# Kernel tuning notes

Measured on AMD Instinct MI355X. Metric: run time of the kernel, lower is better.

## Reference

```python
import jax, jax.numpy as jnp
import numpy as np

D_MODEL = 1024
M = 64            # oscillators; state dim N = 2*M
N = 2 * M
N_H = 2           # Householder reflections per step
DT = 0.1
OMEGA_MAX = 100.0
BATCH, SEQ = 8, 2048


def setup_inputs() -> dict:
    key = jax.random.key(0)
    ks = jax.random.split(key, 8)
    u = jax.random.normal(ks[0], (BATCH, SEQ, D_MODEL), jnp.float32)
    # learned parameters (scaled like the module's small-gain init)
    W_A = jax.random.normal(ks[1], (M, D_MODEL), jnp.float32) * 0.01
    b_A = jnp.zeros((M,), jnp.float32)
    W_k = jax.random.normal(ks[2], (N_H, N, D_MODEL), jnp.float32) * 0.02
    b_k = jnp.zeros((N_H, N), jnp.float32)
    W_beta = jax.random.normal(ks[3], (N_H, D_MODEL), jnp.float32) * 0.02
    b_beta = jnp.zeros((N_H,), jnp.float32)
    B_w = jax.random.normal(ks[4], (N, D_MODEL), jnp.float32) * 0.02
    B_b = jnp.zeros((N,), jnp.float32)
    C = jax.random.normal(ks[5], (D_MODEL, N), jnp.float32) * 0.01
    D = jax.random.normal(ks[6], (D_MODEL,), jnp.float32) * 0.01
    return dict(u=u, W_A=W_A, b_A=b_A, W_k=W_k, b_k=b_k,
                W_beta=W_beta, b_beta=b_beta, B_w=B_w, B_b=B_b, C=C, D=D)


def reference(u, W_A, b_A, W_k, b_k, W_beta, b_beta, B_w, B_b, C, D):
    batch = u.shape[0]
    # --- precompute all input-dependent per-step quantities as big GEMMs ---
    A = jax.nn.relu(jnp.einsum('btd,md->btm', u, W_A) + b_A)
    A = jnp.minimum(A, OMEGA_MAX)                       # clamp(max=omega_max)
    S = 1.0 / (1.0 + (DT * DT) * A)                     # (B,T,M)
    K = jnp.einsum('btd,jnd->btjn', u, W_k) + b_k       # (B,T,n_h,N)
    K = K / jnp.maximum(jnp.linalg.norm(K, axis=-1, keepdims=True), 1e-12)
    beta = 2.0 * jax.nn.sigmoid(jnp.einsum('btd,jd->btj', u, W_beta) + b_beta)
    Bt = jnp.einsum('btd,nd->btn', u, B_w) + B_b        # (B,T,N)

    # time-major for scan
    xs = (jnp.moveaxis(A, 1, 0), jnp.moveaxis(S, 1, 0), jnp.moveaxis(K, 1, 0),
          jnp.moveaxis(beta, 1, 0), jnp.moveaxis(Bt, 1, 0))
    h0 = jnp.zeros((batch, N), u.dtype)

    def step(h, x):
        A_t, S_t, K_t, beta_t, B_t = x
        # oscillatory rotation-contraction R_t @ h (m 2x2 blocks)
        z, y = h[:, :M], h[:, M:]
        z_new = S_t * z - DT * A_t * S_t * y
        y_new = DT * S_t * z + S_t * y
        h = jnp.concatenate([z_new, y_new], axis=-1)
        # sequential Householder product H_t @ h (fixed small n_h loop)
        for j in range(N_H):
            k = K_t[:, j]                                # (B,N), unit norm
            dot = jnp.sum(k * h, axis=-1, keepdims=True)
            h = h - beta_t[:, j:j + 1] * k * dot
        h = h + B_t
        return h, h

    _, hs = jax.lax.scan(step, h0, xs)                  # (T,B,N)
    hs = jnp.moveaxis(hs, 0, 1)                         # (B,T,N)
    return jnp.einsum('btn,dn->btd', hs, C) + u * D
```

## Files before the change

### kernel.cpp

```cpp
#include <hip/hip_runtime.h>
#include <cmath>


#define NTOK 16384
#define TT 2048
#define BB 8
#define DM 1024
#define FS 520
#define CH 64
#define LCH 32
#define NCH 512
#define NW 448
#define NWP 512

typedef short bf16x8 __attribute__((ext_vector_type(8)));
typedef float f32x4 __attribute__((ext_vector_type(4)));

#define GLOAD_LDS16(g, l)                                          \
  __builtin_amdgcn_global_load_lds(                                \
      (const __attribute__((address_space(1))) void*)(g),          \
      (__attribute__((address_space(3))) void*)(l), 16, 0, 0)

__global__ __launch_bounds__(256) void packW(
    const float* __restrict__ W_A, const float* __restrict__ b_A,
    const float* __restrict__ W_k, const float* __restrict__ b_k,
    const float* __restrict__ b_beta,
    const float* __restrict__ B_w, const float* __restrict__ B_b,
    float* __restrict__ Wp, float* __restrict__ bias) {
  int r = blockIdx.x;
  int tid = threadIdx.x;
  const float* src;
  float bv;
  if (r < 64)       { src = W_A + (size_t)r * DM;         bv = b_A[r]; }
  else if (r < 320) { src = W_k + (size_t)(r - 64) * DM;  bv = b_k[r - 64]; }
  else              { src = B_w + (size_t)(r - 320) * DM; bv = B_b[r - 320]; }
  ((float4*)(Wp + (size_t)r * DM))[tid] = ((const float4*)src)[tid];
  if (tid == 0) bias[r] = bv;
  if (r == 0 && tid < 2) bias[448 + tid] = b_beta[tid];
}

__device__ inline unsigned short bf16_rne(float x) {
  unsigned b = __float_as_uint(x);
  b += 0x7FFFu + ((b >> 16) & 1u);
  return (unsigned short)(b >> 16);
}

__device__ inline void split_bf16(float x, unsigned short& h, unsigned short& l) {
  unsigned b = __float_as_uint(x);
  h = (unsigned short)(b >> 16);
  float rem = x - __uint_as_float(b & 0xFFFF0000u);
  l = bf16_rne(rem);
}

__global__ __launch_bounds__(256) void convertU(
    const float* __restrict__ u, unsigned short* __restrict__ uh,
    unsigned short* __restrict__ ul) {
  int gid = blockIdx.x * 256 + threadIdx.x;
  int m = gid >> 8;
  int g = gid & 255;
  float4 v = *(const float4*)(u + (size_t)m * DM + g * 4);
  int kt = g >> 3, gg = g & 7;
  int p = gg & 3, h = gg >> 2;
  int mr = m & 127, mb = m >> 7;
  int pp = p ^ ((mr >> 2) & 3);
  size_t dst = ((size_t)(mb * 32 + kt)) * 4096 + mr * 32 + ((pp << 1) | h) * 4;
  ushort4 hi, lo;
  split_bf16(v.x, hi.x, lo.x);
  split_bf16(v.y, hi.y, lo.y);
  split_bf16(v.z, hi.z, lo.z);
  split_bf16(v.w, hi.w, lo.w);
  *(ushort4*)(uh + dst) = hi;
  *(ushort4*)(ul + dst) = lo;
}

__global__ __launch_bounds__(256) void convertW(
    const float* __restrict__ Wp, unsigned short* __restrict__ Wb) {
  int gid = blockIdx.x * 256 + threadIdx.x;
  int n = gid >> 8, g = gid & 255;
  int kt = g >> 3, gg = g & 7;
  int p = gg & 3, h = gg >> 2;
  int nr = n & 127, nb = n >> 7;
  int pp = p ^ ((nr >> 2) & 3);
  size_t dst = ((size_t)(nb * 32 + kt)) * 4096 + nr * 32 + ((pp << 1) | h) * 4;
  ushort4 hv = make_ushort4(0, 0, 0, 0);
  if (n < NW) {
    float4 v = *(const float4*)(Wp + (size_t)n * DM + g * 4);
    hv.x = bf16_rne(v.x); hv.y = bf16_rne(v.y);
    hv.z = bf16_rne(v.z); hv.w = bf16_rne(v.w);
  }
  *(ushort4*)(Wb + dst) = hv;
}

__global__ __launch_bounds__(256) void convertC(
    const float* __restrict__ Cm, unsigned short* __restrict__ Chp,
    unsigned short* __restrict__ Clp) {
  int gid = blockIdx.x * 256 + threadIdx.x;
  int d = gid >> 5;
  int g = gid & 31;
  float4 v = *(const float4*)(Cm + (size_t)d * 128 + g * 4);
  int kt = g >> 3, gg = g & 7;
  int p = gg & 3, h = gg >> 2;
  int nr = d & 127, nb = d >> 7;
  int pp = p ^ ((nr >> 2) & 3);
  size_t dst = ((size_t)(nb * 4 + kt)) * 4096 + nr * 32 + ((pp << 1) | h) * 4;
  ushort4 hi, lo;
  split_bf16(v.x, hi.x, lo.x);
  split_bf16(v.y, hi.y, lo.y);
  split_bf16(v.z, hi.z, lo.z);
  split_bf16(v.w, hi.w, lo.w);
  *(ushort4*)(Chp + dst) = hi;
  *(ushort4*)(Clp + dst) = lo;
}

__global__ __launch_bounds__(256) void gemmA_mfma(
    const unsigned short* __restrict__ uh, const unsigned short* __restrict__ ul,
    const unsigned short* __restrict__ Wb, float* __restrict__ Feat) {
  __shared__ __align__(16) unsigned short As[8192];
  __shared__ __align__(16) unsigned short Bs[8192];
  const int tid = threadIdx.x;
  const int wv = tid >> 6, ln = tid & 63;
  const int lr = ln & 15, G = ln >> 4;
  const int wm = wv >> 1, wn = wv & 1;
  const int x = G ^ (lr >> 2);
  f32x4 acc[4][4];
#pragma unroll
  for (int i = 0; i < 4; ++i)
#pragma unroll
    for (int j = 0; j < 4; ++j) acc[i][j] = (f32x4){0.f, 0.f, 0.f, 0.f};

  const size_t aBase = (size_t)blockIdx.x * 32 * 4096;
  const size_t bBase = (size_t)blockIdx.y * 32 * 4096;
  const int so = wv * 512 + ln * 8;
  const int ld = wv * 512;

  auto stage = [&](int step, int buf) {
    const unsigned short* pa = (step < 32) ? uh : ul;
    const int kt = step & 31;
    const unsigned short* ga = pa + aBase + (size_t)kt * 4096;
    const unsigned short* gb = Wb + bBase + (size_t)kt * 4096;
    unsigned short* A = As + buf * 4096;
    unsigned short* B = Bs + buf * 4096;
    GLOAD_LDS16(ga + so,        A + ld);
    GLOAD_LDS16(ga + 2048 + so, A + 2048 + ld);
    GLOAD_LDS16(gb + so,        B + ld);
    GLOAD_LDS16(gb + 2048 + so, B + 2048 + ld);
  };

  stage(0, 0);
  __syncthreads();
  for (int s = 0; s < 64; ++s) {
    const int cur = s & 1;
    if (s + 1 < 64) stage(s + 1, cur ^ 1);
    bf16x8 af[4], bfr[4];
    const char* Ab = (const char*)(As + cur * 4096) + ((wm * 64 + lr) << 6) + (x << 4);
    const char* Bb = (const char*)(Bs + cur * 4096) + ((wn * 64 + lr) << 6) + (x << 4);
#pragma unroll
    for (int i = 0; i < 4; ++i) {
      af[i]  = *(const bf16x8*)(Ab + i * 1024);
      bfr[i] = *(const bf16x8*)(Bb + i * 1024);
    }
#pragma unroll
    for (int i = 0; i < 4; ++i)
#pragma unroll
      for (int j = 0; j < 4; ++j)
        acc[i][j] = __builtin_amdgcn_mfma_f32_16x16x32_bf16(
            af[i], bfr[j], acc[i][j], 0, 0, 0);
    __syncthreads();
  }
  const int row0 = (blockIdx.x << 7) + wm * 64 + (G << 2);
  const int col0 = (blockIdx.y << 7) + wn * 64 + lr;
  float* fb = Feat + (size_t)row0 * FS + col0;
#pragma unroll
  for (int i = 0; i < 4; ++i)
#pragma unroll
    for (int j = 0; j < 4; ++j) {
      float* d = fb + (size_t)(i * 16) * FS + j * 16;
#pragma unroll
      for (int r = 0; r < 4; ++r) d[(size_t)r * FS] = acc[i][j][r];
    }
}

__global__ __launch_bounds__(256) void gemmC_mfma(
    const unsigned short* __restrict__ hsh, const unsigned short* __restrict__ hsl,
    const unsigned short* __restrict__ Chp, const unsigned short* __restrict__ Clp,
    const float* __restrict__ u, const float* __restrict__ Dv,
    float* __restrict__ out) {
  __shared__ __align__(16) unsigned short As[8192];
  __shared__ __align__(16) unsigned short Bs[8192];
  const int tid = threadIdx.x;
  const int wv = tid >> 6, ln = tid & 63;
  const int lr = ln & 15, G = ln >> 4;
  const int wm = wv >> 1, wn = wv & 1;
  const int x = G ^ (lr >> 2);
  f32x4 acc[4][4];
#pragma unroll
  for (int i = 0; i < 4; ++i)
#pragma unroll
    for (int j = 0; j < 4; ++j) acc[i][j] = (f32x4){0.f, 0.f, 0.f, 0.f};

  const size_t aBase = (size_t)blockIdx.x * 4 * 4096;
  const size_t bBase = (size_t)blockIdx.y * 4 * 4096;
  const int so = wv * 512 + ln * 8;
  const int ld = wv * 512;

  auto stage = [&](int step, int buf) {
    const int pass = step >> 2, kt = step & 3;
    const unsigned short* pa = (pass == 1) ? hsl : hsh;
    const unsigned short* pb = (pass == 2) ? Clp : Chp;
    const unsigned short* ga = pa + aBase + (size_t)kt * 4096;
    const unsigned short* gb = pb + bBase + (size_t)kt * 4096;
    unsigned short* A = As + buf * 4096;
    unsigned short* B = Bs + buf * 4096;
    GLOAD_LDS16(ga + so,        A + ld);
    GLOAD_LDS16(ga + 2048 + so, A + 2048 + ld);
    GLOAD_LDS16(gb + so,        B + ld);
    GLOAD_LDS16(gb + 2048 + so, B + 2048 + ld);
  };

  stage(0, 0);
  __syncthreads();
  for (int s = 0; s < 12; ++s) {
    const int cur = s & 1;
    if (s + 1 < 12) stage(s + 1, cur ^ 1);
    bf16x8 af[4], bfr[4];
    const char* Ab = (const char*)(As + cur * 4096) + ((wm * 64 + lr) << 6) + (x << 4);
    const char* Bb = (const char*)(Bs + cur * 4096) + ((wn * 64 + lr) << 6) + (x << 4);
#pragma unroll
    for (int i = 0; i < 4; ++i) {
      af[i]  = *(const bf16x8*)(Ab + i * 1024);
      bfr[i] = *(const bf16x8*)(Bb + i * 1024);
    }
#pragma unroll
    for (int i = 0; i < 4; ++i)
#pragma unroll
      for (int j = 0; j < 4; ++j)
        acc[i][j] = __builtin_amdgcn_mfma_f32_16x16x32_bf16(
            af[i], bfr[j], acc[i][j], 0, 0, 0);
    __syncthreads();
  }
  const int row0 = (blockIdx.x << 7) + wm * 64 + (G << 2);
  const int col0 = (blockIdx.y << 7) + wn * 64 + lr;
#pragma unroll
  for (int j = 0; j < 4; ++j) {
    float dv = Dv[col0 + j * 16];
#pragma unroll
    for (int i = 0; i < 4; ++i) {
#pragma unroll
      for (int r = 0; r < 4; ++r) {
        size_t off = (size_t)(row0 + i * 16 + r) * DM + col0 + j * 16;
        out[off] = fmaf(u[off], dv, acc[i][j][r]);
      }
    }
  }
}

__device__ inline float wave_sum(float v) {
#pragma unroll
  for (int off = 32; off > 0; off >>= 1) v += __shfl_xor(v, off, 64);
  return v;
}

__global__ __launch_bounds__(64) void postA(float* __restrict__ Feat,
                                            const float* __restrict__ bias,
                                            const float* __restrict__ u,
                                            const float* __restrict__ Wb) {
  const int t = blockIdx.x, lane = threadIdx.x;
  float* f = Feat + (size_t)t * FS;
  float s0 = 0.f, s1 = 0.f;
#pragma unroll
  for (int j = 0; j < 4; ++j) {
    float4 uv = *(const float4*)(u + (size_t)t * DM + j * 256 + lane * 4);
    float4 w0 = *(const float4*)(Wb + j * 256 + lane * 4);
    float4 w1 = *(const float4*)(Wb + DM + j * 256 + lane * 4);
    s0 = fmaf(uv.x, w0.x, s0); s0 = fmaf(uv.y, w0.y, s0);
    s0 = fmaf(uv.z, w0.z, s0); s0 = fmaf(uv.w, w0.w, s0);
    s1 = fmaf(uv.x, w1.x, s1); s1 = fmaf(uv.y, w1.y, s1);
    s1 = fmaf(uv.z, w1.z, s1); s1 = fmaf(uv.w, w1.w, s1);
  }
  s0 = wave_sum(s0); s1 = wave_sum(s1);
  float a = f[lane] + bias[lane];
  a = fminf(fmaxf(a, 0.f), 100.f);
  float S = 1.f / (1.f + 0.01f * a);
  f[lane] = S;
  f[448 + lane] = 0.1f * a * S;
  float k10 = f[64 + lane] + bias[64 + lane];
  float k11 = f[128 + lane] + bias[128 + lane];
  float n1 = wave_sum(k10 * k10 + k11 * k11);
  float inv1 = 1.f / fmaxf(sqrtf(n1), 1e-12f);
  k10 *= inv1; k11 *= inv1;
  f[64 + lane] = k10; f[128 + lane] = k11;
  float k20 = f[192 + lane] + bias[192 + lane];
  float k21 = f[256 + lane] + bias[256 + lane];
  float n2 = wave_sum(k20 * k20 + k21 * k21);
  float inv2 = 1.f / fmaxf(sqrtf(n2), 1e-12f);
  k20 *= inv2; k21 *= inv2;
  f[192 + lane] = k20; f[256 + lane] = k21;
  float c12 = wave_sum(k10 * k20 + k11 * k21);
  if (lane == 0) {
    f[512] = 2.f / (1.f + expf(-(s0 + bias[448])));
    f[513] = 2.f / (1.f + expf(-(s1 + bias[449])));
    f[514] = c12;
  }
  f[320 + lane] += bias[320 + lane];
  f[384 + lane] += bias[384 + lane];
}

__global__ __launch_bounds__(1024, 8) void scanB1(
    const float* __restrict__ Feat, float* __restrict__ Mc) {
  const int cid = blockIdx.x;
  const int t0 = (cid >> 6) * TT + (cid & 63) * LCH;
  const int tid = threadIdx.x;
  const int col = tid >> 3, q = tid & 7;
  const int i0 = q * 8;
  __shared__ float fb[2][4 * FS];
  float mz[8], my[8];
#pragma unroll
  for (int j = 0; j < 8; ++j) {
    mz[j] = (i0 + j == col) ? 1.f : 0.f;
    my[j] = (64 + i0 + j == col) ? 1.f : 0.f;
  }
  {
    const float4* src = (const float4*)(Feat + (size_t)t0 * FS);
    if (tid < FS) ((float4*)fb[0])[tid] = src[tid];
  }
  __syncthreads();
  for (int g = 0; g < LCH / 4; ++g) {
    const int cur = g & 1;
    float4 pf0;
    const bool pre = (g < LCH / 4 - 1) && (tid < FS);
    if (pre) {
      const float4* src = (const float4*)(Feat + (size_t)(t0 + (g + 1) * 4) * FS);
      pf0 = src[tid];
    }
#pragma unroll
    for (int s = 0; s < 4; ++s) {
      const float* f = fb[cur] + s * FS;
      float sj[8], cj[8], k1z[8], k1y[8], k2z[8], k2y[8];
#pragma unroll
      for (int v = 0; v < 2; ++v) {
        *(float4*)&sj[4 * v]  = *(const float4*)(f + i0 + 4 * v);
        *(float4*)&cj[4 * v]  = *(const float4*)(f + 448 + i0 + 4 * v);
        *(float4*)&k1z[4 * v] = *(const float4*)(f + 64 + i0 + 4 * v);
        *(float4*)&k1y[4 * v] = *(const float4*)(f + 128 + i0 + 4 * v);
        *(float4*)&k2z[4 * v] = *(const float4*)(f + 192 + i0 + 4 * v);
        *(float4*)&k2y[4 * v] = *(const float4*)(f + 256 + i0 + 4 * v);
      }
      float4 sc = *(const float4*)(f + 512);
      float p0 = 0.f, p1 = 0.f, r0 = 0.f, r1 = 0.f;
#pragma unroll
      for (int j = 0; j < 8; ++j) {
        float s0 = sj[j], c1 = cj[j];
        float z = mz[j], y = my[j];
        float sz = s0 * z;
        z = fmaf(-c1, y, sz);
        y = fmaf(s0, y, 0.1f * sz);
        mz[j] = z; my[j] = y;
        if (j & 1) {
          p1 = fmaf(k1z[j], z, p1); p1 = fmaf(k1y[j], y, p1);
          r1 = fmaf(k2z[j], z, r1); r1 = fmaf(k2y[j], y, r1);
        } else {
          p0 = fmaf(k1z[j], z, p0); p0 = fmaf(k1y[j], y, p0);
          r0 = fmaf(k2z[j], z, r0); r0 = fmaf(k2y[j], y, r0);
        }
      }
      float p = p0 + p1, r2 = r0 + r1;
      p  += __shfl_xor(p, 1, 64);  p  += __shfl_xor(p, 2, 64);
      p  += __shfl_xor(p, 4, 64);
      r2 += __shfl_xor(r2, 1, 64); r2 += __shfl_xor(r2, 2, 64);
      r2 += __shfl_xor(r2, 4, 64);
      float e1 = sc.x * p;
      float e2 = sc.y * fmaf(-sc.z, e1, r2);
#pragma unroll
      for (int j = 0; j < 8; ++j) {
        float z = fmaf(-e1, k1z[j], mz[j]);
        mz[j] = fmaf(-e2, k2z[j], z);
        float y = fmaf(-e1, k1y[j], my[j]);
        my[j] = fmaf(-e2, k2y[j], y);
      }
    }
    if (pre) ((float4*)fb[1 - cur])[tid] = pf0;
    __syncthreads();
  }
  float* dst = Mc + ((size_t)cid * 128 + col) * 128;
  *(float4*)(dst + i0)          = *(float4*)&mz[0];
  *(float4*)(dst + i0 + 4)      = *(float4*)&mz[4];
  *(float4*)(dst + 64 + i0)     = *(float4*)&my[0];
  *(float4*)(dst + 64 + i0 + 4) = *(float4*)&my[4];
}

__global__ __launch_bounds__(64) void scanB0(
    const float* __restrict__ Feat, float* __restrict__ dc) {
  const int cid = blockIdx.x;
  const int lane = threadIdx.x;
  float z = 0.f, y = 0.f;
  const int t0 = (cid >> 6) * TT + (cid & 63) * LCH;
  for (int t = t0; t < t0 + LCH; ++t) {
    const float* __restrict__ f = Feat + (size_t)t * FS;
    float s = f[lane], c1 = f[448 + lane];
    float k1z = f[64 + lane], k1y = f[128 + lane];
    float k2z = f[192 + lane], k2y = f[256 + lane];
    float bz = f[320 + lane], by = f[384 + lane];
    float b1 = f[512], b2 = f[513], c12 = f[514];
    float sz = s * z;
    float zn = fmaf(-c1, y, sz);
    float yn = fmaf(s, y, 0.1f * sz);
    float p = fmaf(k1y, yn, k1z * zn);
    float qq = fmaf(k2y, yn, k2z * zn);
#pragma unroll
    for (int off = 32; off > 0; off >>= 1) {
      p += __shfl_xor(p, off, 64);
      qq += __shfl_xor(qq, off, 64);
    }
    float e1 = b1 * p;
    float d2 = fmaf(-c12, e1, qq);
    float e2 = b2 * d2;
    z = fmaf(-e1, k1z, zn); z = fmaf(-e2, k2z, z); z += bz;
    y = fmaf(-e1, k1y, yn); y = fmaf(-e2, k2y, y); y += by;
  }
  dc[(size_t)cid * 128 + lane] = z;
  dc[(size_t)cid * 128 + 64 + lane] = y;
}

__global__ __launch_bounds__(1024, 8) void scanB2(
    const float* __restrict__ Mc, const float* __restrict__ dc,
    float* __restrict__ hstart) {
  const int b = blockIdx.x;
  const int tid = threadIdx.x;
  const int i = tid & 127, jh = tid >> 7;
  __shared__ float h[128];
  __shared__ float red[8][128];
  if (tid < 128) h[tid] = 0.f;
  __syncthreads();
  float mreg[16];
  {
    const float* M0 = Mc + (size_t)(b * CH) * 16384;
#pragma unroll
    for (int j = 0; j < 16; ++j) mreg[j] = M0[(size_t)(jh * 16 + j) * 128 + i];
  }
  for (int c = 0; c < CH; ++c) {
    if (tid < 128) hstart[(size_t)(b * CH + c) * 128 + tid] = h[tid];
    float acc = 0.f;
#pragma unroll
    for (int j = 0; j < 16; ++j) acc = fmaf(mreg[j], h[jh * 16 + j], acc);
    red[jh][i] = acc;
    if (c + 1 < CH) {
      const float* Mn = Mc + (size_t)(b * CH + c + 1) * 16384;
#pragma unroll
      for (int j = 0; j < 16; ++j) mreg[j] = Mn[(size_t)(jh * 16 + j) * 128 + i];
    }
    __syncthreads();
    if (tid < 128) {
      float sum = dc[(size_t)(b * CH + c) * 128 + tid];
#pragma unroll
      for (int k = 0; k < 8; ++k) sum += red[k][tid];
      h[tid] = sum;
    }
    __syncthreads();
  }
}

__global__ __launch_bounds__(64) void scanB3(
    const float* __restrict__ Feat, const float* __restrict__ hstart,
    unsigned short* __restrict__ hsh, unsigned short* __restrict__ hsl) {
  const int cid = blockIdx.x;
  const int lane = threadIdx.x;
  float z = hstart[(size_t)cid * 128 + lane];
  float y = hstart[(size_t)cid * 128 + 64 + lane];
  const int t0 = (cid >> 6) * TT + (cid & 63) * LCH;
  const int ktz = lane >> 5, kkz = lane & 31;
  const int kty = (64 + lane) >> 5;
  const int pz = (kkz >> 2) & 3, hz = kkz >> 4;
  const int lowz = kkz & 3;
  for (int t = t0; t < t0 + LCH; ++t) {
    const float* __restrict__ f = Feat + (size_t)t * FS;
    float s = f[lane], c1 = f[448 + lane];
    float k1z = f[64 + lane], k1y = f[128 + lane];
    float k2z = f[192 + lane], k2y = f[256 + lane];
    float bz = f[320 + lane], by = f[384 + lane];
    float b1 = f[512], b2 = f[513], c12 = f[514];
    float sz = s * z;
    float zn = fmaf(-c1, y, sz);
    float yn = fmaf(s, y, 0.1f * sz);
    float p = fmaf(k1y, yn, k1z * zn);
    float qq = fmaf(k2y, yn, k2z * zn);
#pragma unroll
    for (int off = 32; off > 0; off >>= 1) {
      p += __shfl_xor(p, off, 64);
      qq += __shfl_xor(qq, off, 64);
    }
    float e1 = b1 * p;
    float d2 = fmaf(-c12, e1, qq);
    float e2 = b2 * d2;
    zn = fmaf(-e1, k1z, zn); zn = fmaf(-e2, k2z, zn); zn += bz;
    yn = fmaf(-e1, k1y, yn); yn = fmaf(-e2, k2y, yn); yn += by;
    {
      const int mb = t >> 7, mr = t & 127;
      const int xr = (mr >> 2) & 3;
      size_t idxz = ((size_t)(mb * 4 + ktz)) * 4096 + mr * 32 +
                    ((((pz ^ xr) << 1) | hz)) * 4 + lowz;
      size_t idxy = ((size_t)(mb * 4 + kty)) * 4096 + mr * 32 +
                    ((((pz ^ xr) << 1) | hz)) * 4 + lowz;
      unsigned short hi, lo;
      split_bf16(zn, hi, lo);
      hsh[idxz] = hi; hsl[idxz] = lo;
      split_bf16(yn, hi, lo);
      hsh[idxy] = hi; hsl[idxy] = lo;
    }
    z = zn; y = yn;
  }
}

extern "C" void kernel_launch(void* const* d_in, const int* in_sizes, int n_in,
                              void* d_out, int out_size, void* d_ws, size_t ws_size,
                              hipStream_t stream) {
  const float* u      = (const float*)d_in[0];
  const float* W_A    = (const float*)d_in[1];
  const float* b_A    = (const float*)d_in[2];
  const float* W_k    = (const float*)d_in[3];
  const float* b_k    = (const float*)d_in[4];
  const float* W_beta = (const float*)d_in[5];
  const float* b_beta = (const float*)d_in[6];
  const float* B_w    = (const float*)d_in[7];
  const float* B_b    = (const float*)d_in[8];
  const float* Cm     = (const float*)d_in[9];
  const float* Dv     = (const float*)d_in[10];
  float* out = (float*)d_out;
  char* ws = (char*)d_ws;
  float* Wp     = (float*)(ws);
  unsigned short* Wb = (unsigned short*)(ws + 1835008);
  float* bias   = (float*)(ws + 4194304);
  float* Feat   = (float*)(ws + 4198400);
  unsigned short* uh = (unsigned short*)(ws + 38277120);
  float* Mc     = (float*)(ws + 38277120);
  unsigned short* ul = (unsigned short*)(ws + 71831552);
  unsigned short* hsh = (unsigned short*)(ws + 71831552);
  unsigned short* hsl = (unsigned short*)(ws + 76025856);
  unsigned short* Chp = (unsigned short*)(ws + 80220160);
  unsigned short* Clp = (unsigned short*)(ws + 80482304);
  float* dcv    = (float*)(ws + 80744448);
  float* hstart = (float*)(ws + 81006592);

  packW<<<dim3(448), dim3(256), 0, stream>>>(W_A, b_A, W_k, b_k, b_beta,
                                             B_w, B_b, Wp, bias);
  convertW<<<dim3(512), dim3(256), 0, stream>>>(Wp, Wb);
  convertU<<<dim3(16384), dim3(256), 0, stream>>>(u, uh, ul);
  gemmA_mfma<<<dim3(128, 4), dim3(256), 0, stream>>>(uh, ul, Wb, Feat);
  convertC<<<dim3(128), dim3(256), 0, stream>>>(Cm, Chp, Clp);
  postA<<<dim3(16384), dim3(64), 0, stream>>>(Feat, bias, u, W_beta);
  scanB1<<<dim3(NCH), dim3(1024), 0, stream>>>(Feat, Mc);
  scanB0<<<dim3(NCH), dim3(64), 0, stream>>>(Feat, dcv);
  scanB2<<<dim3(8), dim3(1024), 0, stream>>>(Mc, dcv, hstart);
  scanB3<<<dim3(NCH), dim3(64), 0, stream>>>(Feat, hstart, hsh, hsl);
  gemmC_mfma<<<dim3(128, 8), dim3(256), 0, stream>>>(hsh, hsl, Chp, Clp,
                                                     u, Dv, out);
}
```

Baseline: 429.4 us.

## Fuse chunk-offset scan into transition-matrix kernel and prefetch in carry scan

```diff
diff --git a/kernel.cpp b/kernel.cpp
--- a/kernel.cpp
+++ b/kernel.cpp
@@ -20,6 +20,13 @@
   __builtin_amdgcn_global_load_lds(                                \
       (const __attribute__((address_space(1))) void*)(g),          \
       (__attribute__((address_space(3))) void*)(l), 16, 0, 0)
+
+#define RAW_BAR() do {                                             \
+    asm volatile("s_waitcnt lgkmcnt(0)" ::: "memory");             \
+    __builtin_amdgcn_sched_barrier(0);                             \
+    __builtin_amdgcn_s_barrier();                                  \
+    __builtin_amdgcn_sched_barrier(0);                             \
+  } while (0)
 
 __global__ __launch_bounds__(256) void packW(
     const float* __restrict__ W_A, const float* __restrict__ b_A,
@@ -305,14 +312,50 @@
   f[384 + lane] += bias[384 + lane];
 }
 
-__global__ __launch_bounds__(1024, 8) void scanB1(
-    const float* __restrict__ Feat, float* __restrict__ Mc) {
-  const int cid = blockIdx.x;
+__global__ __launch_bounds__(1024, 8) void scanB01(
+    const float* __restrict__ Feat, float* __restrict__ Mc,
+    float* __restrict__ dc) {
+  const int bid = blockIdx.x;
+  const int tid = threadIdx.x;
+  __shared__ float fb[2][4 * FS];
+
+  if (bid < NCH / 16) {
+    const int cid = bid * 16 + (tid >> 6);
+    const int lane = tid & 63;
+    float z = 0.f, y = 0.f;
+    const int t0 = (cid >> 6) * TT + (cid & 63) * LCH;
+    for (int t = t0; t < t0 + LCH; ++t) {
+      const float* __restrict__ f = Feat + (size_t)t * FS;
+      float s = f[lane], c1 = f[448 + lane];
+      float k1z = f[64 + lane], k1y = f[128 + lane];
+      float k2z = f[192 + lane], k2y = f[256 + lane];
+      float bz = f[320 + lane], by = f[384 + lane];
+      float b1 = f[512], b2 = f[513], c12 = f[514];
+      float sz = s * z;
+      float zn = fmaf(-c1, y, sz);
+      float yn = fmaf(s, y, 0.1f * sz);
+      float p = fmaf(k1y, yn, k1z * zn);
+      float qq = fmaf(k2y, yn, k2z * zn);
+#pragma unroll
+      for (int off = 32; off > 0; off >>= 1) {
+        p += __shfl_xor(p, off, 64);
+        qq += __shfl_xor(qq, off, 64);
+      }
+      float e1 = b1 * p;
+      float d2 = fmaf(-c12, e1, qq);
+      float e2 = b2 * d2;
+      z = fmaf(-e1, k1z, zn); z = fmaf(-e2, k2z, z); z += bz;
+      y = fmaf(-e1, k1y, yn); y = fmaf(-e2, k2y, y); y += by;
+    }
+    dc[(size_t)cid * 128 + lane] = z;
+    dc[(size_t)cid * 128 + 64 + lane] = y;
+    return;
+  }
+
+  const int cid = bid - NCH / 16;
   const int t0 = (cid >> 6) * TT + (cid & 63) * LCH;
-  const int tid = threadIdx.x;
   const int col = tid >> 3, q = tid & 7;
   const int i0 = q * 8;
-  __shared__ float fb[2][4 * FS];
   float mz[8], my[8];
 #pragma unroll
   for (int j = 0; j < 8; ++j) {
@@ -388,39 +431,6 @@
   *(float4*)(dst + 64 + i0 + 4) = *(float4*)&my[4];
 }
 
-__global__ __launch_bounds__(64) void scanB0(
-    const float* __restrict__ Feat, float* __restrict__ dc) {
-  const int cid = blockIdx.x;
-  const int lane = threadIdx.x;
-  float z = 0.f, y = 0.f;
-  const int t0 = (cid >> 6) * TT + (cid & 63) * LCH;
-  for (int t = t0; t < t0 + LCH; ++t) {
-    const float* __restrict__ f = Feat + (size_t)t * FS;
-    float s = f[lane], c1 = f[448 + lane];
-    float k1z = f[64 + lane], k1y = f[128 + lane];
-    float k2z = f[192 + lane], k2y = f[256 + lane];
-    float bz = f[320 + lane], by = f[384 + lane];
-    float b1 = f[512], b2 = f[513], c12 = f[514];
-    float sz = s * z;
-    float zn = fmaf(-c1, y, sz);
-    float yn = fmaf(s, y, 0.1f * sz);
-    float p = fmaf(k1y, yn, k1z * zn);
-    float qq = fmaf(k2y, yn, k2z * zn);
-#pragma unroll
-    for (int off = 32; off > 0; off >>= 1) {
-      p += __shfl_xor(p, off, 64);
-      qq += __shfl_xor(qq, off, 64);
-    }
-    float e1 = b1 * p;
-    float d2 = fmaf(-c12, e1, qq);
-    float e2 = b2 * d2;
-    z = fmaf(-e1, k1z, zn); z = fmaf(-e2, k2z, z); z += bz;
-    y = fmaf(-e1, k1y, yn); y = fmaf(-e2, k2y, y); y += by;
-  }
-  dc[(size_t)cid * 128 + lane] = z;
-  dc[(size_t)cid * 128 + 64 + lane] = y;
-}
-
 __global__ __launch_bounds__(1024, 8) void scanB2(
     const float* __restrict__ Mc, const float* __restrict__ dc,
     float* __restrict__ hstart) {
@@ -431,31 +441,37 @@
   __shared__ float red[8][128];
   if (tid < 128) h[tid] = 0.f;
   __syncthreads();
-  float mreg[16];
+  float ma[16], mb[16];
+  float d0 = 0.f, d1 = 0.f;
   {
     const float* M0 = Mc + (size_t)(b * CH) * 16384;
 #pragma unroll
-    for (int j = 0; j < 16; ++j) mreg[j] = M0[(size_t)(jh * 16 + j) * 128 + i];
+    for (int j = 0; j < 16; ++j) ma[j] = M0[(size_t)(jh * 16 + j) * 128 + i];
+    if (tid < 128) d0 = dc[(size_t)(b * CH) * 128 + tid];
   }
   for (int c = 0; c < CH; ++c) {
+    if (c + 1 < CH) {
+      const float* Mn = Mc + (size_t)(b * CH + c + 1) * 16384;
+#pragma unroll
+      for (int j = 0; j < 16; ++j) mb[j] = Mn[(size_t)(jh * 16 + j) * 128 + i];
+      if (tid < 128) d1 = dc[(size_t)(b * CH + c + 1) * 128 + tid];
+    }
     if (tid < 128) hstart[(size_t)(b * CH + c) * 128 + tid] = h[tid];
     float acc = 0.f;
 #pragma unroll
-    for (int j = 0; j < 16; ++j) acc = fmaf(mreg[j], h[jh * 16 + j], acc);
+    for (int j = 0; j < 16; ++j) acc = fmaf(ma[j], h[jh * 16 + j], acc);
     red[jh][i] = acc;
-    if (c + 1 < CH) {
-      const float* Mn = Mc + (size_t)(b * CH + c + 1) * 16384;
-#pragma unroll
-      for (int j = 0; j < 16; ++j) mreg[j] = Mn[(size_t)(jh * 16 + j) * 128 + i];
-    }
-    __syncthreads();
+    RAW_BAR();
     if (tid < 128) {
-      float sum = dc[(size_t)(b * CH + c) * 128 + tid];
+      float sum = d0;
 #pragma unroll
       for (int k = 0; k < 8; ++k) sum += red[k][tid];
       h[tid] = sum;
     }
-    __syncthreads();
+    RAW_BAR();
+#pragma unroll
+    for (int j = 0; j < 16; ++j) ma[j] = mb[j];
+    d0 = d1;
   }
 }
 
@@ -547,8 +563,7 @@
   gemmA_mfma<<<dim3(128, 4), dim3(256), 0, stream>>>(uh, ul, Wb, Feat);
   convertC<<<dim3(128), dim3(256), 0, stream>>>(Cm, Chp, Clp);
   postA<<<dim3(16384), dim3(64), 0, stream>>>(Feat, bias, u, W_beta);
-  scanB1<<<dim3(NCH), dim3(1024), 0, stream>>>(Feat, Mc);
-  scanB0<<<dim3(NCH), dim3(64), 0, stream>>>(Feat, dcv);
+  scanB01<<<dim3(NCH / 16 + NCH), dim3(1024), 0, stream>>>(Feat, Mc, dcv);
   scanB2<<<dim3(8), dim3(1024), 0, stream>>>(Mc, dcv, hstart);
   scanB3<<<dim3(NCH), dim3(64), 0, stream>>>(Feat, hstart, hsh, hsl);
   gemmC_mfma<<<dim3(128, 8), dim3(256), 0, stream>>>(hsh, hsl, Chp, Clp,
```

After: 546.5 us. +27.3%, slower.
